# Optimization experiments

Measured on AMD Instinct MI355X. Metric: run time of the kernel, lower is better.

## Reference

```python
import jax, jax.numpy as jnp
import numpy as np

B = 131072
D_IN = 128
D_H = 128
DT = 1.0
LN_EPS = 1e-5


def setup_inputs() -> dict:
    key = jax.random.key(0)
    ks = jax.random.split(key, 12)
    s_in = 1.0 / np.sqrt(D_IN)
    s_h = 1.0 / np.sqrt(D_H)
    s_g = 1.0 / np.sqrt(D_IN + D_H)
    return {
        "x_t": jax.random.normal(ks[0], (B, D_IN), dtype=jnp.float32),
        "state": jax.random.normal(ks[1], (B, D_H), dtype=jnp.float32),
        "w_in": jax.random.uniform(ks[2], (D_H, D_IN), jnp.float32, -s_in, s_in),
        "b_in": jax.random.uniform(ks[3], (D_H,), jnp.float32, -s_in, s_in),
        "w_rec": jax.random.uniform(ks[4], (D_H, D_H), jnp.float32, -s_h, s_h),
        "w_gate": jax.random.uniform(ks[5], (D_H, D_IN + D_H), jnp.float32, -s_g, s_g),
        "b_gate": jax.random.uniform(ks[6], (D_H,), jnp.float32, -s_g, s_g),
        "bias": jnp.zeros((D_H,), jnp.float32),
        "log_step": jnp.zeros((D_H,), jnp.float32),
        "ln_gamma": jnp.ones((D_IN + D_H,), jnp.float32),
        "ln_beta": jnp.zeros((D_IN + D_H,), jnp.float32),
    }


def reference(x_t, state, w_in, b_in, w_rec, w_gate, b_gate, bias, log_step, ln_gamma, ln_beta):
    # per-unit learned time scale in (0, 1)
    step_size = jax.nn.sigmoid(log_step)  # [D_H]
    # drive = input_proj(x) + recurrent_proj(tanh(state)) + bias
    drive = (jnp.einsum("bi,hi->bh", x_t, w_in) + b_in
             + jnp.einsum("bj,hj->bh", jnp.tanh(state), w_rec)
             + bias)  # [B, D_H]
    # LayerNorm over concat([x, state])
    gi = jnp.concatenate([x_t, state], axis=-1)  # [B, D_IN+D_H]
    mu = jnp.mean(gi, axis=-1, keepdims=True)
    var = jnp.mean(jnp.square(gi - mu), axis=-1, keepdims=True)
    gi = (gi - mu) * jax.lax.rsqrt(var + LN_EPS) * ln_gamma + ln_beta
    gate = jax.nn.sigmoid(jnp.einsum("bk,hk->bh", gi, w_gate) + b_gate)  # [B, D_H]
    target = jnp.tanh(drive)
    blend = jnp.minimum(DT * step_size * gate, 1.0)
    new_state = state + blend * (target - state)
    return new_state
```

## Files before the change

### kernel.cpp

```cpp
#include <hip/hip_runtime.h>

#define D        128
#define M_TILE   32
#define THREADS  512
#define B_ROWS   131072
#define NTILES   (B_ROWS / M_TILE)
#define GRID_BLOCKS 512

typedef __bf16  bf16x8  __attribute__((ext_vector_type(8)));
typedef float   f32x4   __attribute__((ext_vector_type(4)));

#define LOG2E 1.4426950408889634f

__device__ __forceinline__ float fexp2(float x) { return __builtin_amdgcn_exp2f(x); }
__device__ __forceinline__ float frcp(float x)  { return __builtin_amdgcn_rcpf(x); }

__device__ __forceinline__ float fast_tanh(float x) {
    float e = fexp2(x * (2.f * LOG2E));
    return 1.f - 2.f * frcp(e + 1.f);
}
__device__ __forceinline__ float fast_sigmoid(float x) {
    return frcp(1.f + fexp2(-LOG2E * x));
}

__global__ __launch_bounds__(THREADS, 4)
void liquid_cell(const float* __restrict__ x,      const float* __restrict__ st,
                 const float* __restrict__ w_in,   const float* __restrict__ b_in,
                 const float* __restrict__ w_rec,  const float* __restrict__ w_gate,
                 const float* __restrict__ b_gate, const float* __restrict__ bias,
                 const float* __restrict__ log_step,
                 const float* __restrict__ gamma,  const float* __restrict__ beta,
                 float* __restrict__ out)
{
    __shared__ __align__(16) __bf16 A1[M_TILE * 256];
    __shared__ __align__(16) __bf16 A2[M_TILE * 256];
    __shared__ __align__(16) float  SBUF[M_TILE * 128];

    const int tid  = threadIdx.x;
    const int lane = tid & 63;
    const int wave = tid >> 6;
    const int q    = lane >> 4;
    const int arow = lane & 15;
    const int hcol = wave * 16 + arow;
    const int koff = q * 8;

    const float stepv = fast_sigmoid(log_step[hcol]);
    const float bd    = b_in[hcol] + bias[hcol];
    float       bg    = b_gate[hcol];

    bf16x8 wd[8], wg[8];
    float betaAcc = 0.f;
    #pragma unroll
    for (int kb = 0; kb < 8; ++kb) {
        const int k = kb * 32 + koff;
        const float* s1 = (k < 128) ? (w_in  + hcol * 128 + k)
                                    : (w_rec + hcol * 128 + (k - 128));
        const float* s2 = w_gate + hcol * 256 + k;
        #pragma unroll
        for (int j = 0; j < 8; ++j) {
            wd[kb][j] = (__bf16)s1[j];
            const float wv = s2[j];
            wg[kb][j] = (__bf16)(wv * gamma[k + j]);
            betaAcc  += wv * beta[k + j];
        }
    }
    betaAcc += __shfl_xor(betaAcc, 16);
    betaAcc += __shfl_xor(betaAcc, 32);
    bg += betaAcc;

    const int r   = tid >> 4;
    const int c0  = (tid & 15) * 8;
    const int sw  = (r & 7) << 3;
    const int swf = (r & 7) << 2;
    const int rsw = (arow & 7) << 3;

    for (int tile = blockIdx.x; tile < NTILES; tile += GRID_BLOCKS) {
        const float* xp = x  + ((long)tile * M_TILE + r) * D + c0;
        const float* sp = st + ((long)tile * M_TILE + r) * D + c0;
        const f32x4 xa = *(const f32x4*)xp, xb = *(const f32x4*)(xp + 4);
        const f32x4 sa = *(const f32x4*)sp, sb = *(const f32x4*)(sp + 4);

        float sum = 0.f, sq = 0.f;
        #pragma unroll
        for (int j = 0; j < 4; ++j) {
            sum += xa[j] + xb[j] + sa[j] + sb[j];
            sq  += xa[j]*xa[j] + xb[j]*xb[j] + sa[j]*sa[j] + sb[j]*sb[j];
        }
        #pragma unroll
        for (int m = 1; m < 16; m <<= 1) {
            sum += __shfl_xor(sum, m);
            sq  += __shfl_xor(sq,  m);
        }
        const float mu   = sum * (1.f / 256.f);
        const float rstd = __builtin_amdgcn_rsqf(sq * (1.f / 256.f) - mu * mu + 1e-5f);
        const float nmur = -mu * rstd;

        bf16x8 a1x, a1s, a2x, a2s;
        #pragma unroll
        for (int j = 0; j < 4; ++j) {
            a1x[j]     = (__bf16)xa[j];
            a1x[j + 4] = (__bf16)xb[j];
            a1s[j]     = (__bf16)fast_tanh(sa[j]);
            a1s[j + 4] = (__bf16)fast_tanh(sb[j]);
            a2x[j]     = (__bf16)(xa[j] * rstd + nmur);
            a2x[j + 4] = (__bf16)(xb[j] * rstd + nmur);
            a2s[j]     = (__bf16)(sa[j] * rstd + nmur);
            a2s[j + 4] = (__bf16)(sb[j] * rstd + nmur);
        }

        __syncthreads();
        *(bf16x8*)&A1[(r * 256 +       c0) ^ sw] = a1x;
        *(bf16x8*)&A1[(r * 256 + 128 + c0) ^ sw] = a1s;
        *(bf16x8*)&A2[(r * 256 +       c0) ^ sw] = a2x;
        *(bf16x8*)&A2[(r * 256 + 128 + c0) ^ sw] = a2s;
        *(f32x4*)&SBUF[(r * 128 + c0)     ^ swf] = sa;
        *(f32x4*)&SBUF[(r * 128 + c0 + 4) ^ swf] = sb;
        __syncthreads();

        f32x4 acc1[2], acc2[2];
        #pragma unroll
        for (int ms = 0; ms < 2; ++ms) { acc1[ms] = (f32x4)(0.f); acc2[ms] = (f32x4)(0.f); }

        #pragma unroll
        for (int ms = 0; ms < 2; ++ms) {
            const int base = (ms * 16 + arow) * 256;
            #pragma unroll
            for (int kb = 0; kb < 8; ++kb) {
                bf16x8 a = *(const bf16x8*)&A1[base + ((kb * 32 + koff) ^ rsw)];
                acc1[ms] = __builtin_amdgcn_mfma_f32_16x16x32_bf16(a, wd[kb], acc1[ms], 0, 0, 0);
            }
            #pragma unroll
            for (int kb = 0; kb < 8; ++kb) {
                bf16x8 a = *(const bf16x8*)&A2[base + ((kb * 32 + koff) ^ rsw)];
                acc2[ms] = __builtin_amdgcn_mfma_f32_16x16x32_bf16(a, wg[kb], acc2[ms], 0, 0, 0);
            }
        }

        const long obase = (long)tile * M_TILE;
        #pragma unroll
        for (int ms = 0; ms < 2; ++ms) {
            #pragma unroll
            for (int rg = 0; rg < 4; ++rg) {
                const int row = ms * 16 + q * 4 + rg;
                const float s      = SBUF[(row * 128 + hcol) ^ ((row & 7) << 2)];
                const float target = fast_tanh(acc1[ms][rg] + bd);
                const float gate   = fast_sigmoid(acc2[ms][rg] + bg);
                const float blend  = fminf(stepv * gate, 1.f);
                out[(obase + row) * D + hcol] = s + blend * (target - s);
            }
        }
    }
}

extern "C" void kernel_launch(void* const* d_in, const int* in_sizes, int n_in,
                              void* d_out, int out_size, void* d_ws, size_t ws_size,
                              hipStream_t stream) {
    const float* x        = (const float*)d_in[0];
    const float* st       = (const float*)d_in[1];
    const float* w_in     = (const float*)d_in[2];
    const float* b_in     = (const float*)d_in[3];
    const float* w_rec    = (const float*)d_in[4];
    const float* w_gate   = (const float*)d_in[5];
    const float* b_gate   = (const float*)d_in[6];
    const float* bias     = (const float*)d_in[7];
    const float* log_step = (const float*)d_in[8];
    const float* gamma    = (const float*)d_in[9];
    const float* beta     = (const float*)d_in[10];
    float* out = (float*)d_out;

    hipLaunchKernelGGL(liquid_cell, dim3(GRID_BLOCKS), dim3(THREADS), 0, stream,
                       x, st, w_in, b_in, w_rec, w_gate, b_gate, bias,
                       log_step, gamma, beta, out);
}
```

Baseline: 66.59 us.

## Prefetch next tile of x and state into LDS with global_load_lds

Replaces the direct per-thread global loads of x and state with asynchronous global-to-LDS loads into a staging buffer. The first tile is issued before the weight setup, and the next tile is issued right after the A-operand writes, so it can overlap with the MFMA and epilogue work. The aim is to hide global load latency in this bandwidth-bound loop. It adds 32KB of LDS per block, which can lower the number of resident blocks. It also relies on correct waitcnt handling for the LDS DMA across the barrier.

New measurement: 115.3 us. 73.2% more time.

```diff
diff --git a/kernel.cpp b/kernel.cpp
--- a/kernel.cpp
+++ b/kernel.cpp
@@ -1,4 +1,5 @@
 #include <hip/hip_runtime.h>
+#include <stdint.h>
 
 #define D        128
 #define M_TILE   32
@@ -21,6 +22,13 @@
 }
 __device__ __forceinline__ float fast_sigmoid(float x) {
     return frcp(1.f + fexp2(-LOG2E * x));
+}
+
+typedef __attribute__((address_space(1))) const void g_as_t;
+typedef __attribute__((address_space(3))) void       l_as_t;
+
+__device__ __forceinline__ void gload_lds16(const float* g, float* l) {
+    __builtin_amdgcn_global_load_lds((g_as_t*)g, (l_as_t*)l, 16, 0, 0);
 }
 
 __global__ __launch_bounds__(THREADS, 4)
@@ -35,6 +43,7 @@
     __shared__ __align__(16) __bf16 A1[M_TILE * 256];
     __shared__ __align__(16) __bf16 A2[M_TILE * 256];
     __shared__ __align__(16) float  SBUF[M_TILE * 128];
+    __shared__ __align__(16) float  STAGE[2 * M_TILE * 128];
 
     const int tid  = threadIdx.x;
     const int lane = tid & 63;
@@ -43,6 +52,19 @@
     const int arow = lane & 15;
     const int hcol = wave * 16 + arow;
     const int koff = q * 8;
+
+    {
+        const long tbase = (long)blockIdx.x * (M_TILE * D);
+        #pragma unroll
+        for (int c = 0; c < 4; ++c) {
+            const int m     = wave + c * 8;
+            const int part  = (m < 16) ? 0 : 1;
+            const int ibase = (part ? (m - 16) : m) * 256;
+            const int i     = ibase + lane * 4;
+            const int src   = i ^ (((i >> 7) & 7) << 2);
+            gload_lds16((part ? st : x) + tbase + src, &STAGE[part * 4096 + ibase]);
+        }
+    }
 
     const float stepv = fast_sigmoid(log_step[hcol]);
     const float bd    = b_in[hcol] + bias[hcol];
@@ -68,17 +90,21 @@
     betaAcc += __shfl_xor(betaAcc, 32);
     bg += betaAcc;
 
-    const int r   = tid >> 4;
-    const int c0  = (tid & 15) * 8;
-    const int sw  = (r & 7) << 3;
-    const int swf = (r & 7) << 2;
-    const int rsw = (arow & 7) << 3;
+    const int r    = tid >> 4;
+    const int c0   = (tid & 15) * 8;
+    const int sw   = (r & 7) << 3;
+    const int swf  = (r & 7) << 2;
+    const int rsw  = (arow & 7) << 3;
+    const int sx0  = (r * 128 + c0) ^ swf;
+    const int sx1  = (r * 128 + c0 + 4) ^ swf;
 
     for (int tile = blockIdx.x; tile < NTILES; tile += GRID_BLOCKS) {
-        const float* xp = x  + ((long)tile * M_TILE + r) * D + c0;
-        const float* sp = st + ((long)tile * M_TILE + r) * D + c0;
-        const f32x4 xa = *(const f32x4*)xp, xb = *(const f32x4*)(xp + 4);
-        const f32x4 sa = *(const f32x4*)sp, sb = *(const f32x4*)(sp + 4);
+        __syncthreads();
+
+        const f32x4 xa = *(const f32x4*)&STAGE[sx0];
+        const f32x4 xb = *(const f32x4*)&STAGE[sx1];
+        const f32x4 sa = *(const f32x4*)&STAGE[4096 + sx0];
+        const f32x4 sb = *(const f32x4*)&STAGE[4096 + sx1];
 
         float sum = 0.f, sq = 0.f;
         #pragma unroll
@@ -108,14 +134,28 @@
             a2s[j + 4] = (__bf16)(sb[j] * rstd + nmur);
         }
 
-        __syncthreads();
         *(bf16x8*)&A1[(r * 256 +       c0) ^ sw] = a1x;
         *(bf16x8*)&A1[(r * 256 + 128 + c0) ^ sw] = a1s;
         *(bf16x8*)&A2[(r * 256 +       c0) ^ sw] = a2x;
         *(bf16x8*)&A2[(r * 256 + 128 + c0) ^ sw] = a2s;
         *(f32x4*)&SBUF[(r * 128 + c0)     ^ swf] = sa;
         *(f32x4*)&SBUF[(r * 128 + c0 + 4) ^ swf] = sb;
+
         __syncthreads();
+
+        const int next = tile + GRID_BLOCKS;
+        if (next < NTILES) {
+            const long tbase = (long)next * (M_TILE * D);
+            #pragma unroll
+            for (int c = 0; c < 4; ++c) {
+                const int m     = wave + c * 8;
+                const int part  = (m < 16) ? 0 : 1;
+                const int ibase = (part ? (m - 16) : m) * 256;
+                const int i     = ibase + lane * 4;
+                const int src   = i ^ (((i >> 7) & 7) << 2);
+                gload_lds16((part ? st : x) + tbase + src, &STAGE[part * 4096 + ibase]);
+            }
+        }
 
         f32x4 acc1[2], acc2[2];
         #pragma unroll
```

## Precompute weight fragments in prep kernel, stream them per tile, prefetch next inputs

Applied to the files above, without the earlier changes.

A small prep kernel converts the weights to bf16 MFMA fragments (gamma folded in) and computes the per-column parameters into the workspace. The main kernel then reloads fragments from global or L2 each tile instead of holding 16 fragment registers, which lowers register pressure so occupancy can rise to 6 blocks with 768 blocks in the grid. It also prefetches the next tile's x and state into registers while the MFMAs run. In exchange it adds a second launch and extra fragment loads per tile, and falls back to the old kernel when the workspace is too small.

After: 217.8 us. +227.2%, slower.

```diff
diff --git a/kernel.cpp b/kernel.cpp
--- a/kernel.cpp
+++ b/kernel.cpp
@@ -5,12 +5,16 @@
 #define THREADS  512
 #define B_ROWS   131072
 #define NTILES   (B_ROWS / M_TILE)
-#define GRID_BLOCKS 512
+#define GRID_MAIN 768
+#define GRID_FB   512
 
 typedef __bf16  bf16x8  __attribute__((ext_vector_type(8)));
 typedef float   f32x4   __attribute__((ext_vector_type(4)));
 
 #define LOG2E 1.4426950408889634f
+#define WS_FRAGS   4096
+#define WS_PARAMS_OFF (2 * WS_FRAGS)
+#define WS_NEEDED  (2 * WS_FRAGS * 16 + 128 * 16)
 
 __device__ __forceinline__ float fexp2(float x) { return __builtin_amdgcn_exp2f(x); }
 __device__ __forceinline__ float frcp(float x)  { return __builtin_amdgcn_rcpf(x); }
@@ -23,14 +27,200 @@
     return frcp(1.f + fexp2(-LOG2E * x));
 }
 
+__global__ __launch_bounds__(THREADS)
+void prep(const float* __restrict__ w_in,   const float* __restrict__ b_in,
+          const float* __restrict__ w_rec,  const float* __restrict__ w_gate,
+          const float* __restrict__ b_gate, const float* __restrict__ bias,
+          const float* __restrict__ log_step,
+          const float* __restrict__ gamma,  const float* __restrict__ beta,
+          bf16x8* __restrict__ ws)
+{
+    const int bid = blockIdx.x, tid = threadIdx.x;
+    if (bid < 8) {
+        const int t    = bid * THREADS + tid;
+        const int l    = t & 63;
+        const int kb   = (t >> 6) & 7;
+        const int w    = (t >> 9) & 7;
+        const int hcol = w * 16 + (l & 15);
+        const int k    = kb * 32 + ((l >> 4) & 3) * 8;
+        bf16x8 fd, fg;
+        const float* s1 = (k < 128) ? (w_in + hcol * 128 + k) : (w_rec + hcol * 128 + (k - 128));
+        const float* s2 = w_gate + hcol * 256 + k;
+        #pragma unroll
+        for (int j = 0; j < 8; ++j) {
+            fd[j] = (__bf16)s1[j];
+            fg[j] = (__bf16)(s2[j] * gamma[k + j]);
+        }
+        ws[t]            = fd;
+        ws[WS_FRAGS + t] = fg;
+    } else {
+        const int h   = tid >> 2;
+        const int sub = tid & 3;
+        float acc = 0.f;
+        const float* wp = w_gate + h * 256 + sub * 64;
+        const float* bp = beta + sub * 64;
+        #pragma unroll
+        for (int k = 0; k < 64; k += 4) {
+            const f32x4 wv = *(const f32x4*)(wp + k);
+            const f32x4 bv = *(const f32x4*)(bp + k);
+            acc += wv[0]*bv[0] + wv[1]*bv[1] + wv[2]*bv[2] + wv[3]*bv[3];
+        }
+        acc += __shfl_xor(acc, 1);
+        acc += __shfl_xor(acc, 2);
+        if (sub == 0) {
+            f32x4 p;
+            p[0] = fast_sigmoid(log_step[h]);
+            p[1] = b_in[h] + bias[h];
+            p[2] = b_gate[h] + acc;
+            p[3] = 0.f;
+            *((f32x4*)(ws + WS_PARAMS_OFF) + h) = p;
+        }
+    }
+}
+
+__global__ __launch_bounds__(THREADS, 6)
+void liquid_cell(const float* __restrict__ x, const float* __restrict__ st,
+                 const bf16x8* __restrict__ ws, float* __restrict__ out)
+{
+    __shared__ __align__(16) __bf16 A1[M_TILE * 256];
+    __shared__ __align__(16) __bf16 A2[M_TILE * 256];
+    __shared__ __align__(16) float  SBUF[M_TILE * 128];
+
+    const int tid  = threadIdx.x;
+    const int lane = tid & 63;
+    const int wave = tid >> 6;
+    const int q    = lane >> 4;
+    const int arow = lane & 15;
+    const int hcol = wave * 16 + arow;
+    const int koff = q * 8;
+    const int fbase = wave * 512 + lane;
+
+    const f32x4 pp  = *((const f32x4*)(ws + WS_PARAMS_OFF) + hcol);
+    const float stepv = pp[0], bd = pp[1], bg = pp[2];
+
+    const int r    = tid >> 4;
+    const int c0   = (tid & 15) * 8;
+    const int sw   = (r & 7) << 3;
+    const int swf  = (r & 7) << 2;
+    const int rsw  = (arow & 7) << 3;
+
+    const bf16x8* WD = ws;
+    const bf16x8* WG = ws + WS_FRAGS;
+
+    f32x4 xa, xb, sa, sb;
+    {
+        const float* xp = x  + ((long)blockIdx.x * M_TILE + r) * D + c0;
+        const float* sp = st + ((long)blockIdx.x * M_TILE + r) * D + c0;
+        xa = *(const f32x4*)xp;  xb = *(const f32x4*)(xp + 4);
+        sa = *(const f32x4*)sp;  sb = *(const f32x4*)(sp + 4);
+    }
+
+    for (int tile = blockIdx.x; tile < NTILES; tile += GRID_MAIN) {
+        float sum = 0.f, sq = 0.f;
+        #pragma unroll
+        for (int j = 0; j < 4; ++j) {
+            sum += xa[j] + xb[j] + sa[j] + sb[j];
+            sq  += xa[j]*xa[j] + xb[j]*xb[j] + sa[j]*sa[j] + sb[j]*sb[j];
+        }
+        #pragma unroll
+        for (int m = 1; m < 16; m <<= 1) {
+            sum += __shfl_xor(sum, m);
+            sq  += __shfl_xor(sq,  m);
+        }
+        const float mu   = sum * (1.f / 256.f);
+        const float rstd = __builtin_amdgcn_rsqf(sq * (1.f / 256.f) - mu * mu + 1e-5f);
+        const float nmur = -mu * rstd;
+
+        bf16x8 a1x, a1s, a2x, a2s;
+        #pragma unroll
+        for (int j = 0; j < 4; ++j) {
+            a1x[j]     = (__bf16)xa[j];
+            a1x[j + 4] = (__bf16)xb[j];
+            a1s[j]     = (__bf16)fast_tanh(sa[j]);
+            a1s[j + 4] = (__bf16)fast_tanh(sb[j]);
+            a2x[j]     = (__bf16)(xa[j] * rstd + nmur);
+            a2x[j + 4] = (__bf16)(xb[j] * rstd + nmur);
+            a2s[j]     = (__bf16)(sa[j] * rstd + nmur);
+            a2s[j + 4] = (__bf16)(sb[j] * rstd + nmur);
+        }
+
+        __syncthreads();
+        *(bf16x8*)&A1[(r * 256 +       c0) ^ sw] = a1x;
+        *(bf16x8*)&A1[(r * 256 + 128 + c0) ^ sw] = a1s;
+        *(bf16x8*)&A2[(r * 256 +       c0) ^ sw] = a2x;
+        *(bf16x8*)&A2[(r * 256 + 128 + c0) ^ sw] = a2s;
+        *(f32x4*)&SBUF[(r * 128 + c0)     ^ swf] = sa;
+        *(f32x4*)&SBUF[(r * 128 + c0 + 4) ^ swf] = sb;
+        __syncthreads();
+
+        bf16x8 fw[8];
+        #pragma unroll
+        for (int kb = 0; kb < 8; ++kb) fw[kb] = WG[fbase + kb * 64];
+
+        const int next = tile + GRID_MAIN;
+        if (next < NTILES) {
+            const float* xpn = x  + ((long)next * M_TILE + r) * D + c0;
+            const float* spn = st + ((long)next * M_TILE + r) * D + c0;
+            xa = *(const f32x4*)xpn;  xb = *(const f32x4*)(xpn + 4);
+            sa = *(const f32x4*)spn;  sb = *(const f32x4*)(spn + 4);
+        }
+
+        f32x4 acc2[2];
+        acc2[0] = (f32x4)(0.f); acc2[1] = (f32x4)(0.f);
+        #pragma unroll
+        for (int ms = 0; ms < 2; ++ms) {
+            const int base = (ms * 16 + arow) * 256;
+            #pragma unroll
+            for (int kb = 0; kb < 8; ++kb) {
+                bf16x8 a = *(const bf16x8*)&A2[base + ((kb * 32 + koff) ^ rsw)];
+                acc2[ms] = __builtin_amdgcn_mfma_f32_16x16x32_bf16(a, fw[kb], acc2[ms], 0, 0, 0);
+            }
+        }
+        float gate[2][4];
+        #pragma unroll
+        for (int ms = 0; ms < 2; ++ms)
+            #pragma unroll
+            for (int rg = 0; rg < 4; ++rg)
+                gate[ms][rg] = fast_sigmoid(acc2[ms][rg] + bg);
+
+        #pragma unroll
+        for (int kb = 0; kb < 8; ++kb) fw[kb] = WD[fbase + kb * 64];
+
+        f32x4 acc1[2];
+        acc1[0] = (f32x4)(0.f); acc1[1] = (f32x4)(0.f);
+        #pragma unroll
+        for (int ms = 0; ms < 2; ++ms) {
+            const int base = (ms * 16 + arow) * 256;
+            #pragma unroll
+            for (int kb = 0; kb < 8; ++kb) {
+                bf16x8 a = *(const bf16x8*)&A1[base + ((kb * 32 + koff) ^ rsw)];
+                acc1[ms] = __builtin_amdgcn_mfma_f32_16x16x32_bf16(a, fw[kb], acc1[ms], 0, 0, 0);
+            }
+        }
+
+        const long obase = (long)tile * M_TILE;
+        #pragma unroll
+        for (int ms = 0; ms < 2; ++ms) {
+            #pragma unroll
+            for (int rg = 0; rg < 4; ++rg) {
+                const int row = ms * 16 + q * 4 + rg;
+                const float s      = SBUF[(row * 128 + hcol) ^ ((row & 7) << 2)];
+                const float target = fast_tanh(acc1[ms][rg] + bd);
+                const float blend  = fminf(stepv * gate[ms][rg], 1.f);
+                out[(obase + row) * D + hcol] = s + blend * (target - s);
+            }
+        }
+    }
+}
+
 __global__ __launch_bounds__(THREADS, 4)
-void liquid_cell(const float* __restrict__ x,      const float* __restrict__ st,
-                 const float* __restrict__ w_in,   const float* __restrict__ b_in,
-                 const float* __restrict__ w_rec,  const float* __restrict__ w_gate,
-                 const float* __restrict__ b_gate, const float* __restrict__ bias,
-                 const float* __restrict__ log_step,
-                 const float* __restrict__ gamma,  const float* __restrict__ beta,
-                 float* __restrict__ out)
+void liquid_cell_fb(const float* __restrict__ x,      const float* __restrict__ st,
+                    const float* __restrict__ w_in,   const float* __restrict__ b_in,
+                    const float* __restrict__ w_rec,  const float* __restrict__ w_gate,
+                    const float* __restrict__ b_gate, const float* __restrict__ bias,
+                    const float* __restrict__ log_step,
+                    const float* __restrict__ gamma,  const float* __restrict__ beta,
+                    float* __restrict__ out)
 {
     __shared__ __align__(16) __bf16 A1[M_TILE * 256];
     __shared__ __align__(16) __bf16 A2[M_TILE * 256];
@@ -68,13 +258,13 @@
     betaAcc += __shfl_xor(betaAcc, 32);
     bg += betaAcc;
 
-    const int r   = tid >> 4;
-    const int c0  = (tid & 15) * 8;
-    const int sw  = (r & 7) << 3;
-    const int swf = (r & 7) << 2;
-    const int rsw = (arow & 7) << 3;
-
-    for (int tile = blockIdx.x; tile < NTILES; tile += GRID_BLOCKS) {
+    const int r    = tid >> 4;
+    const int c0   = (tid & 15) * 8;
+    const int sw   = (r & 7) << 3;
+    const int swf  = (r & 7) << 2;
+    const int rsw  = (arow & 7) << 3;
+
+    for (int tile = blockIdx.x; tile < NTILES; tile += GRID_FB) {
         const float* xp = x  + ((long)tile * M_TILE + r) * D + c0;
         const float* sp = st + ((long)tile * M_TILE + r) * D + c0;
         const f32x4 xa = *(const f32x4*)xp, xb = *(const f32x4*)(xp + 4);
@@ -168,7 +358,16 @@
     const float* beta     = (const float*)d_in[10];
     float* out = (float*)d_out;
 
-    hipLaunchKernelGGL(liquid_cell, dim3(GRID_BLOCKS), dim3(THREADS), 0, stream,
-                       x, st, w_in, b_in, w_rec, w_gate, b_gate, bias,
-                       log_step, gamma, beta, out);
-}
+    if (ws_size >= (size_t)WS_NEEDED) {
+        bf16x8* ws = (bf16x8*)d_ws;
+        hipLaunchKernelGGL(prep, dim3(9), dim3(THREADS), 0, stream,
+                           w_in, b_in, w_rec, w_gate, b_gate, bias,
+                           log_step, gamma, beta, ws);
+        hipLaunchKernelGGL(liquid_cell, dim3(GRID_MAIN), dim3(THREADS), 0, stream,
+                           x, st, ws, out);
+    } else {
+        hipLaunchKernelGGL(liquid_cell_fb, dim3(GRID_FB), dim3(THREADS), 0, stream,
+                           x, st, w_in, b_in, w_rec, w_gate, b_gate, bias,
+                           log_step, gamma, beta, out);
+    }
+}
```

## Fold LayerNorm into gate epilogue, share x tile, prefetch next tile

Applied to the files above, without the earlier changes.

The LayerNorm is applied after the matmul: the raw bf16 x and state are multiplied by gamma-scaled gate weights, then corrected per row with rstd*(acc - mu*colsum). This lets x be staged once for both GEMMs and drops the separate normalized A buffer, cutting shared memory and per-element work. The next tile's global loads are issued before the MFMA section so they overlap with compute. In exchange, state used in the final blend is read back as bf16 rather than fp32, which loses precision in the output. Skipping the centering step can also add cancellation error.

Result: slower. 147.2 us (+121.1%).

```diff
diff --git a/kernel.cpp b/kernel.cpp
--- a/kernel.cpp
+++ b/kernel.cpp
@@ -5,7 +5,7 @@
 #define THREADS  512
 #define B_ROWS   131072
 #define NTILES   (B_ROWS / M_TILE)
-#define GRID_BLOCKS 512
+#define GRID     512
 
 typedef __bf16  bf16x8  __attribute__((ext_vector_type(8)));
 typedef float   f32x4   __attribute__((ext_vector_type(4)));
@@ -32,9 +32,10 @@
                  const float* __restrict__ gamma,  const float* __restrict__ beta,
                  float* __restrict__ out)
 {
-    __shared__ __align__(16) __bf16 A1[M_TILE * 256];
-    __shared__ __align__(16) __bf16 A2[M_TILE * 256];
-    __shared__ __align__(16) float  SBUF[M_TILE * 128];
+    __shared__ __align__(16) __bf16 XT[M_TILE * 128];
+    __shared__ __align__(16) __bf16 TT[M_TILE * 128];
+    __shared__ __align__(16) __bf16 SS[M_TILE * 128];
+    __shared__ float2 MUB[M_TILE];
 
     const int tid  = threadIdx.x;
     const int lane = tid & 63;
@@ -49,7 +50,7 @@
     float       bg    = b_gate[hcol];
 
     bf16x8 wd[8], wg[8];
-    float betaAcc = 0.f;
+    float betaAcc = 0.f, colsum = 0.f;
     #pragma unroll
     for (int kb = 0; kb < 8; ++kb) {
         const int k = kb * 32 + koff;
@@ -60,26 +61,32 @@
         for (int j = 0; j < 8; ++j) {
             wd[kb][j] = (__bf16)s1[j];
             const float wv = s2[j];
-            wg[kb][j] = (__bf16)(wv * gamma[k + j]);
+            const __bf16 g = (__bf16)(wv * gamma[k + j]);
+            wg[kb][j] = g;
+            colsum   += (float)g;
             betaAcc  += wv * beta[k + j];
         }
     }
     betaAcc += __shfl_xor(betaAcc, 16);
     betaAcc += __shfl_xor(betaAcc, 32);
+    colsum  += __shfl_xor(colsum, 16);
+    colsum  += __shfl_xor(colsum, 32);
     bg += betaAcc;
 
-    const int r   = tid >> 4;
-    const int c0  = (tid & 15) * 8;
-    const int sw  = (r & 7) << 3;
-    const int swf = (r & 7) << 2;
-    const int rsw = (arow & 7) << 3;
-
-    for (int tile = blockIdx.x; tile < NTILES; tile += GRID_BLOCKS) {
-        const float* xp = x  + ((long)tile * M_TILE + r) * D + c0;
-        const float* sp = st + ((long)tile * M_TILE + r) * D + c0;
-        const f32x4 xa = *(const f32x4*)xp, xb = *(const f32x4*)(xp + 4);
-        const f32x4 sa = *(const f32x4*)sp, sb = *(const f32x4*)(sp + 4);
-
+    const int r    = tid >> 4;
+    const int c0   = (tid & 15) * 8;
+    const int sw   = (r & 7) << 3;
+    const int rsw  = (arow & 7) << 3;
+
+    f32x4 xa, xb, sa, sb;
+    {
+        const float* xp = x  + ((long)blockIdx.x * M_TILE + r) * D + c0;
+        const float* sp = st + ((long)blockIdx.x * M_TILE + r) * D + c0;
+        xa = *(const f32x4*)xp;  xb = *(const f32x4*)(xp + 4);
+        sa = *(const f32x4*)sp;  sb = *(const f32x4*)(sp + 4);
+    }
+
+    for (int tile = blockIdx.x; tile < NTILES; tile += GRID) {
         float sum = 0.f, sq = 0.f;
         #pragma unroll
         for (int j = 0; j < 4; ++j) {
@@ -93,59 +100,87 @@
         }
         const float mu   = sum * (1.f / 256.f);
         const float rstd = __builtin_amdgcn_rsqf(sq * (1.f / 256.f) - mu * mu + 1e-5f);
-        const float nmur = -mu * rstd;
-
-        bf16x8 a1x, a1s, a2x, a2s;
+
+        bf16x8 fx, ft, fs;
         #pragma unroll
         for (int j = 0; j < 4; ++j) {
-            a1x[j]     = (__bf16)xa[j];
-            a1x[j + 4] = (__bf16)xb[j];
-            a1s[j]     = (__bf16)fast_tanh(sa[j]);
-            a1s[j + 4] = (__bf16)fast_tanh(sb[j]);
-            a2x[j]     = (__bf16)(xa[j] * rstd + nmur);
-            a2x[j + 4] = (__bf16)(xb[j] * rstd + nmur);
-            a2s[j]     = (__bf16)(sa[j] * rstd + nmur);
-            a2s[j + 4] = (__bf16)(sb[j] * rstd + nmur);
+            fx[j]     = (__bf16)xa[j];
+            fx[j + 4] = (__bf16)xb[j];
+            ft[j]     = (__bf16)fast_tanh(sa[j]);
+            ft[j + 4] = (__bf16)fast_tanh(sb[j]);
+            fs[j]     = (__bf16)sa[j];
+            fs[j + 4] = (__bf16)sb[j];
         }
 
         __syncthreads();
-        *(bf16x8*)&A1[(r * 256 +       c0) ^ sw] = a1x;
-        *(bf16x8*)&A1[(r * 256 + 128 + c0) ^ sw] = a1s;
-        *(bf16x8*)&A2[(r * 256 +       c0) ^ sw] = a2x;
-        *(bf16x8*)&A2[(r * 256 + 128 + c0) ^ sw] = a2s;
-        *(f32x4*)&SBUF[(r * 128 + c0)     ^ swf] = sa;
-        *(f32x4*)&SBUF[(r * 128 + c0 + 4) ^ swf] = sb;
+        *(bf16x8*)&XT[(r * 128 + c0) ^ sw] = fx;
+        *(bf16x8*)&TT[(r * 128 + c0) ^ sw] = ft;
+        *(bf16x8*)&SS[(r * 128 + c0) ^ sw] = fs;
+        if ((tid & 15) == 0) MUB[r] = make_float2(mu, rstd);
         __syncthreads();
 
-        f32x4 acc1[2], acc2[2];
-        #pragma unroll
-        for (int ms = 0; ms < 2; ++ms) { acc1[ms] = (f32x4)(0.f); acc2[ms] = (f32x4)(0.f); }
-
-        #pragma unroll
-        for (int ms = 0; ms < 2; ++ms) {
-            const int base = (ms * 16 + arow) * 256;
-            #pragma unroll
-            for (int kb = 0; kb < 8; ++kb) {
-                bf16x8 a = *(const bf16x8*)&A1[base + ((kb * 32 + koff) ^ rsw)];
-                acc1[ms] = __builtin_amdgcn_mfma_f32_16x16x32_bf16(a, wd[kb], acc1[ms], 0, 0, 0);
-            }
-            #pragma unroll
-            for (int kb = 0; kb < 8; ++kb) {
-                bf16x8 a = *(const bf16x8*)&A2[base + ((kb * 32 + koff) ^ rsw)];
+        const int next = tile + GRID;
+        if (next < NTILES) {
+            const float* xpn = x  + ((long)next * M_TILE + r) * D + c0;
+            const float* spn = st + ((long)next * M_TILE + r) * D + c0;
+            xa = *(const f32x4*)xpn;  xb = *(const f32x4*)(xpn + 4);
+            sa = *(const f32x4*)spn;  sb = *(const f32x4*)(spn + 4);
+        }
+
+        f32x4 acc2[2];
+        acc2[0] = (f32x4)(0.f); acc2[1] = (f32x4)(0.f);
+        #pragma unroll
+        for (int ms = 0; ms < 2; ++ms) {
+            const int base = (ms * 16 + arow) * 128;
+            #pragma unroll
+            for (int kb = 0; kb < 4; ++kb) {
+                bf16x8 a = *(const bf16x8*)&XT[base + ((kb * 32 + koff) ^ rsw)];
                 acc2[ms] = __builtin_amdgcn_mfma_f32_16x16x32_bf16(a, wg[kb], acc2[ms], 0, 0, 0);
             }
-        }
-
-        const long obase = (long)tile * M_TILE;
+            #pragma unroll
+            for (int kb = 4; kb < 8; ++kb) {
+                bf16x8 a = *(const bf16x8*)&SS[base + (((kb - 4) * 32 + koff) ^ rsw)];
+                acc2[ms] = __builtin_amdgcn_mfma_f32_16x16x32_bf16(a, wg[kb], acc2[ms], 0, 0, 0);
+            }
+        }
+
+        float gate[2][4];
         #pragma unroll
         for (int ms = 0; ms < 2; ++ms) {
             #pragma unroll
             for (int rg = 0; rg < 4; ++rg) {
                 const int row = ms * 16 + q * 4 + rg;
-                const float s      = SBUF[(row * 128 + hcol) ^ ((row & 7) << 2)];
+                const float2 mr = MUB[row];
+                gate[ms][rg] = fast_sigmoid(mr.y * (acc2[ms][rg] - mr.x * colsum) + bg);
+            }
+        }
+
+        f32x4 acc1[2];
+        acc1[0] = (f32x4)(0.f); acc1[1] = (f32x4)(0.f);
+        #pragma unroll
+        for (int ms = 0; ms < 2; ++ms) {
+            const int base = (ms * 16 + arow) * 128;
+            #pragma unroll
+            for (int kb = 0; kb < 4; ++kb) {
+                bf16x8 a = *(const bf16x8*)&XT[base + ((kb * 32 + koff) ^ rsw)];
+                acc1[ms] = __builtin_amdgcn_mfma_f32_16x16x32_bf16(a, wd[kb], acc1[ms], 0, 0, 0);
+            }
+            #pragma unroll
+            for (int kb = 4; kb < 8; ++kb) {
+                bf16x8 a = *(const bf16x8*)&TT[base + (((kb - 4) * 32 + koff) ^ rsw)];
+                acc1[ms] = __builtin_amdgcn_mfma_f32_16x16x32_bf16(a, wd[kb], acc1[ms], 0, 0, 0);
+            }
+        }
+
+        const long obase = (long)tile * M_TILE;
+        #pragma unroll
+        for (int ms = 0; ms < 2; ++ms) {
+            #pragma unroll
+            for (int rg = 0; rg < 4; ++rg) {
+                const int row = ms * 16 + q * 4 + rg;
+                const float s      = (float)SS[(row * 128 + hcol) ^ ((row & 7) << 3)];
                 const float target = fast_tanh(acc1[ms][rg] + bd);
-                const float gate   = fast_sigmoid(acc2[ms][rg] + bg);
-                const float blend  = fminf(stepv * gate, 1.f);
+                const float blend  = fminf(stepv * gate[ms][rg], 1.f);
                 out[(obase + row) * D + hcol] = s + blend * (target - s);
             }
         }
@@ -168,7 +203,7 @@
     const float* beta     = (const float*)d_in[10];
     float* out = (float*)d_out;
 
-    hipLaunchKernelGGL(liquid_cell, dim3(GRID_BLOCKS), dim3(THREADS), 0, stream,
+    hipLaunchKernelGGL(liquid_cell, dim3(GRID), dim3(THREADS), 0, stream,
                        x, st, w_in, b_in, w_rec, w_gate, b_gate, bias,
                        log_step, gamma, beta, out);
 }
```
